# Kernel tuning notes

Hardware: AMD Instinct MI355X
Metric: run time of the kernel (lower is better)

Reference implementation:

```python
import jax, jax.numpy as jnp
import numpy as np

B = 32768
H = 512
NH = 8
EPS = 1e-5


def _glorot(key, shape):
    fan_in, fan_out = shape[-1], shape[0]
    lim = (6.0 / (fan_in + fan_out)) ** 0.5
    return jax.random.uniform(key, shape, jnp.float32, -lim, lim)


def setup_inputs() -> dict:
    key = jax.random.key(0)
    ks = jax.random.split(key, 32)
    d = {
        "graph_features": jax.random.normal(ks[0], (B, H), jnp.float32),
        "seq_features": jax.random.normal(ks[1], (B, H), jnp.float32),
        "tabular_features": jax.random.normal(ks[2], (B, H), jnp.float32),
    }
    i = 3
    for name in ("g2s", "s2g", "t2m"):
        d[f"{name}_w_in"] = _glorot(ks[i], (3 * H, H)); i += 1
        d[f"{name}_b_in"] = jnp.zeros((3 * H,), jnp.float32)
        d[f"{name}_w_out"] = _glorot(ks[i], (H, H)); i += 1
        d[f"{name}_b_out"] = jnp.zeros((H,), jnp.float32)
    for name in ("gate_g", "gate_s", "gate_t"):
        d[f"{name}_w"] = _glorot(ks[i], (H, 2 * H)); i += 1
        d[f"{name}_b"] = jnp.zeros((H,), jnp.float32)
    d["fc1_w"] = _glorot(ks[i], (2 * H, 3 * H)); i += 1
    d["fc1_b"] = jnp.zeros((2 * H,), jnp.float32)
    d["ln_g"] = jnp.ones((2 * H,), jnp.float32)
    d["ln_b"] = jnp.zeros((2 * H,), jnp.float32)
    d["fc2_w"] = _glorot(ks[i], (H, 2 * H)); i += 1
    d["fc2_b"] = jnp.zeros((H,), jnp.float32)
    return d


def _mha(q, k, v, w_in, b_in, w_out, b_out):
    # q: [B,Sq,H], k/v: [B,Sk,H]. PyTorch nn.MultiheadAttention math (eval mode).
    dh = H // NH
    qp = q @ w_in[:H].T + b_in[:H]
    kp = k @ w_in[H:2 * H].T + b_in[H:2 * H]
    vp = v @ w_in[2 * H:].T + b_in[2 * H:]
    qh = qp.reshape(qp.shape[0], qp.shape[1], NH, dh)
    kh = kp.reshape(kp.shape[0], kp.shape[1], NH, dh)
    vh = vp.reshape(vp.shape[0], vp.shape[1], NH, dh)
    scores = jnp.einsum("bqhd,bkhd->bhqk", qh, kh) / jnp.sqrt(jnp.float32(dh))
    attn = jax.nn.softmax(scores, axis=-1)
    out = jnp.einsum("bhqk,bkhd->bqhd", attn, vh).reshape(q.shape[0], q.shape[1], H)
    return out @ w_out.T + b_out


def reference(graph_features, seq_features, tabular_features,
              g2s_w_in, g2s_b_in, g2s_w_out, g2s_b_out,
              s2g_w_in, s2g_b_in, s2g_w_out, s2g_b_out,
              t2m_w_in, t2m_b_in, t2m_w_out, t2m_b_out,
              gate_g_w, gate_g_b, gate_s_w, gate_s_b, gate_t_w, gate_t_b,
              fc1_w, fc1_b, ln_g, ln_b, fc2_w, fc2_b):
    g = graph_features[:, None, :]   # [B,1,H]
    s = seq_features[:, None, :]
    t = tabular_features[:, None, :]

    graph_to_seq = _mha(s, g, g, g2s_w_in, g2s_b_in, g2s_w_out, g2s_b_out)
    seq_to_graph = _mha(g, s, s, s2g_w_in, s2g_b_in, s2g_w_out, s2g_b_out)

    graph_gate = jax.nn.sigmoid(jnp.concatenate([g, seq_to_graph], -1) @ gate_g_w.T + gate_g_b)
    seq_gate = jax.nn.sigmoid(jnp.concatenate([s, graph_to_seq], -1) @ gate_s_w.T + gate_s_b)
    gated_graph = g * graph_gate
    gated_seq = s * seq_gate

    multimodal = jnp.concatenate([gated_graph, gated_seq], axis=1)  # [B,2,H]
    t2m = _mha(multimodal, t, t, t2m_w_in, t2m_b_in, t2m_w_out, t2m_b_out)  # [B,2,H]

    tab_comb = jnp.concatenate([t, t2m.mean(axis=1, keepdims=True)], -1)
    tab_gate = jax.nn.sigmoid(tab_comb @ gate_t_w.T + gate_t_b)
    gated_tab = t * tab_gate

    allf = jnp.concatenate([gated_graph[:, 0], gated_seq[:, 0], gated_tab[:, 0]], -1)  # [B,3H]
    h = allf @ fc1_w.T + fc1_b
    mu = h.mean(-1, keepdims=True)
    var = ((h - mu) ** 2).mean(-1, keepdims=True)
    h = (h - mu) / jnp.sqrt(var + EPS) * ln_g + ln_b
    h = jax.nn.relu(h)
    return h @ fc2_w.T + fc2_b
```

## Files before the change

### kernel.cpp

```cpp
#include <hip/hip_runtime.h>
#include <stdint.h>
#include <stddef.h>

#define MROWS 32768
#define HDIM  512
#define CH    16384
#define BM 128
#define BN 128
#define BK 64

typedef __attribute__((ext_vector_type(8))) _Float16 half8;
typedef __attribute__((ext_vector_type(4))) _Float16 half4v;
typedef __attribute__((ext_vector_type(4))) float    f32x4;

static __device__ __forceinline__ void gld_lds16(const void* g, void* l) {
    __builtin_amdgcn_global_load_lds(
        (__attribute__((address_space(1))) void*)(uintptr_t)g,
        (__attribute__((address_space(3))) void*)(uint32_t)(uintptr_t)l,
        16, 0, 0);
}

struct CvtJob  { const float* src; _Float16* dst; int srcld4, dstld, rowlen4, rows; };
struct CvtJobs { CvtJob j[11]; };

__global__ __launch_bounds__(256)
void cvt_rows(CvtJobs J) {
    const CvtJob jb = J.j[blockIdx.y];
    const int row = blockIdx.x;
    if (row >= jb.rows) return;
    const float4* __restrict__ s = (const float4*)jb.src + (size_t)row * jb.srcld4;
    _Float16* __restrict__ d = jb.dst + (size_t)row * jb.dstld;
    for (int c = threadIdx.x; c < jb.rowlen4; c += 256) {
        const float4 v = s[c];
        half4v o = { (_Float16)v.x, (_Float16)v.y, (_Float16)v.z, (_Float16)v.w };
        *(half4v*)(d + c * 4) = o;
    }
}

__global__ __launch_bounds__(384)
void cvt_chunk3(const float* __restrict__ x0, const float* __restrict__ x1,
                const float* __restrict__ x2, _Float16* __restrict__ dst) {
    const int row = blockIdx.x;
    const int mod = threadIdx.x >> 7;
    const int c   = threadIdx.x & 127;
    const float* s = (mod == 0) ? x0 : (mod == 1) ? x1 : x2;
    const float4 v = ((const float4*)(s + (size_t)row * 512))[c];
    half4v o = { (_Float16)v.x, (_Float16)v.y, (_Float16)v.z, (_Float16)v.w };
    *(half4v*)(dst + (size_t)row * 1536 + mod * 512 + c * 4) = o;
}

struct TcvtArgs { const float* src[3]; _Float16* dst; };
__global__ __launch_bounds__(256)
void tcvt512(TcvtArgs a) {
    __shared__ float t[32][33];
    const int m = blockIdx.z;
    const float* __restrict__ src = a.src[m];
    _Float16* __restrict__ dst = a.dst + (size_t)m * HDIM * HDIM;
    const int bx = blockIdx.x * 32, by = blockIdx.y * 32;
    const int tx = threadIdx.x & 31, ty = threadIdx.x >> 5;
    #pragma unroll
    for (int q = 0; q < 4; ++q)
        t[ty + q * 8][tx] = src[(size_t)(by + ty + q * 8) * 512 + bx + tx];
    __syncthreads();
    #pragma unroll
    for (int q = 0; q < 4; ++q)
        dst[(size_t)(bx + ty + q * 8) * 512 + by + tx] = (_Float16)t[tx][ty + q * 8];
}

struct MvArgs { const float* W[3]; const float* x[3]; const float* b[3]; float* y; int ldw, woff; };
__global__ __launch_bounds__(256)
void mv3(MvArgs a) {
    const int m = blockIdx.y;
    const int i = blockIdx.x * 256 + threadIdx.x;
    const float* __restrict__ W = a.W[m] + (size_t)i * a.ldw + a.woff;
    const float* __restrict__ x = a.x[m];
    float s = a.b[m][i];
    for (int j = 0; j < 512; ++j) s += W[j] * x[j];
    a.y[m * 512 + i] = s;
}

struct GemmP {
    const void* A1;
    const _Float16* W; const float* bias; void* C;
    int K, ldA1, ldw, ldc, coff;
    int zsA, zsW, zsC;
};

template<int EPI, int OCC>
__global__ __launch_bounds__(256, OCC)
void gemm_k(GemmP p) {
    __shared__ __align__(16) unsigned char smem[32768];
    _Float16* Asm = (_Float16*)smem;
    _Float16* Bsm = (_Float16*)(smem + 16384);

    const int tid  = threadIdx.x;
    const int wid  = tid >> 6;
    const int lane = tid & 63;
    const int m0 = blockIdx.x * BM;
    const int n0 = blockIdx.y * BN;
    const ptrdiff_t zz = (ptrdiff_t)blockIdx.z;
    const _Float16* __restrict__ A1h = (const _Float16*)((const char*)p.A1 + zz * p.zsA);
    const _Float16* __restrict__ Wp  = (const _Float16*)((const char*)p.W + zz * p.zsW);
    char* Cz = (char*)p.C + zz * p.zsC;

    const int wr = (wid >> 1) * 64;
    const int wc = (wid & 1) * 64;
    const int l15 = lane & 15;
    const int lhi = lane >> 4;

    f32x4 acc[4][4] = {};

    for (int kt = 0; kt < p.K; kt += BK) {
        #pragma unroll
        for (int i = 0; i < 4; ++i) {
            const int seg = wid * 256 + i * 64 + lane;
            const int row = seg >> 3;
            const int ke  = (seg & 7) * 8;
            gld_lds16(Wp  + (size_t)(n0 + row) * p.ldw  + kt + ke, &Bsm[seg * 8]);
            gld_lds16(A1h + (size_t)(m0 + row) * p.ldA1 + kt + ke, &Asm[seg * 8]);
        }
        __syncthreads();
        #pragma unroll
        for (int kk = 0; kk < BK; kk += 32) {
            half8 fa[4], fb[4];
            #pragma unroll
            for (int i = 0; i < 4; ++i) {
                fa[i] = *(const half8*)&Asm[(wr + i * 16 + l15) * BK + kk + lhi * 8];
                fb[i] = *(const half8*)&Bsm[(wc + i * 16 + l15) * BK + kk + lhi * 8];
            }
            #pragma unroll
            for (int i = 0; i < 4; ++i)
                #pragma unroll
                for (int j = 0; j < 4; ++j)
                    acc[i][j] = __builtin_amdgcn_mfma_f32_16x16x32_f16(fa[i], fb[j], acc[i][j], 0, 0, 0);
        }
        __syncthreads();
    }

    if (EPI == 3) {
        float* Cf = (float*)smem;
        float* __restrict__ C = (float*)Cz;
        #pragma unroll
        for (int h = 0; h < 2; ++h) {
            if ((wr >> 6) == h) {
                #pragma unroll
                for (int j = 0; j < 4; ++j) {
                    const int col = wc + j * 16 + l15;
                    const float bia = p.bias ? p.bias[n0 + col] : 0.f;
                    #pragma unroll
                    for (int i = 0; i < 4; ++i)
                        #pragma unroll
                        for (int r = 0; r < 4; ++r)
                            Cf[(i * 16 + lhi * 4 + r) * 128 + col] = acc[i][j][r] + bia;
                }
            }
            __syncthreads();
            #pragma unroll
            for (int pph = 0; pph < 8; ++pph) {
                const int seg = pph * 256 + tid;
                const int row = seg >> 5, cs = seg & 31;
                const float4 v = *(const float4*)&Cf[row * 128 + cs * 4];
                *(float4*)&C[(size_t)(m0 + h * 64 + row) * p.ldc + n0 + cs * 4] = v;
            }
            __syncthreads();
        }
    } else {
        _Float16* Ct = (_Float16*)smem;
        #pragma unroll
        for (int j = 0; j < 4; ++j) {
            const int col = wc + j * 16 + l15;
            const float bia = (EPI == 2) ? 0.f : (p.bias ? p.bias[n0 + col] : 0.f);
            #pragma unroll
            for (int i = 0; i < 4; ++i)
                #pragma unroll
                for (int r = 0; r < 4; ++r) {
                    float v = acc[i][j][r] + bia;
                    if (EPI == 1) v = 1.f / (1.f + __expf(-v));
                    Ct[(wr + i * 16 + lhi * 4 + r) * 128 + col] = (_Float16)v;
                }
        }
        __syncthreads();
        _Float16* __restrict__ C = (_Float16*)Cz;
        #pragma unroll
        for (int pph = 0; pph < 8; ++pph) {
            const int seg = pph * 256 + tid;
            const int row = seg >> 4, cs = seg & 15;
            half8 hv = *(const half8*)&Ct[row * 128 + cs * 8];
            const size_t cidx = (size_t)(m0 + row) * p.ldc + p.coff + n0 + cs * 8;
            if (EPI == 1) {
                const half8 xv = *(const half8*)(A1h + (size_t)(m0 + row) * p.ldA1
                                                 + n0 + cs * 8);
                hv = hv * xv;
            }
            if (EPI == 2) { const half8 old = *(const half8*)&C[cidx]; hv = hv + old; }
            *(half8*)&C[cidx] = hv;
        }
    }
}

struct Gemm8P {
    const _Float16* A; const _Float16* W; const float* bias; void* C;
    int K, ldA, ldW, ldc, coff;
};

template<int EPI>
__global__ __launch_bounds__(512, 1)
void gemm8(Gemm8P p) {
    __shared__ __align__(16) unsigned char lds[131072];
    char* LA = (char*)lds;
    char* LB = (char*)lds + 65536;

    const int tid  = threadIdx.x;
    const int wid  = tid >> 6;
    const int lane = tid & 63;
    const int wm = wid >> 2;
    const int wn = wid & 3;
    const int l15 = lane & 15;
    const int lhi = lane >> 4;
    const int m0 = blockIdx.x * 256;
    const int n0 = blockIdx.y * 256;
    const _Float16* __restrict__ A = p.A;
    const _Float16* __restrict__ W = p.W;
    const int ldA = p.ldA, ldW = p.ldW;
    const int nT = p.K >> 6;

    f32x4 acc[8][4] = {};

    auto stageh = [&](const _Float16* src, int ld, int r0, char* base, int t, int kh) {
        const int q = t & 1;
        const int kt = t * 64 + kh * 32;
        char* dst = base + (size_t)(q * 2 + kh) * 16384;
        #pragma unroll
        for (int k = 0; k < 2; ++k) {
            const int j = tid + k * 512;
            const int row = j >> 2, i = j & 3;
            const int kc = i ^ ((row >> 1) & 3);
            gld_lds16(src + (size_t)(r0 + row) * ld + kt + kc * 8,
                      dst + (size_t)j * 16);
        }
    };
    #define STAGE8(t, kh) { stageh(A, ldA, m0, LA, (t), (kh)); stageh(W, ldW, n0, LB, (t), (kh)); }

    STAGE8(0, 0);
    STAGE8(0, 1);
    if (nT > 1) { STAGE8(1, 0); asm volatile("s_waitcnt vmcnt(8)" ::: "memory"); }
    else        {               asm volatile("s_waitcnt vmcnt(0)" ::: "memory"); }
    __builtin_amdgcn_s_barrier();
    asm volatile("" ::: "memory");

    for (int t = 0; t < nT; ++t) {
        const int q = t & 1;
        #pragma unroll
        for (int kh = 0; kh < 2; ++kh) {
            const char* ra = LA + (size_t)(q * 2 + kh) * 16384;
            const char* rb = LB + (size_t)(q * 2 + kh) * 16384;
            half8 fa[8], fb[4];
            #pragma unroll
            for (int nf = 0; nf < 4; ++nf) {
                const int row = wn * 64 + nf * 16 + l15;
                const int sl = lhi ^ ((row >> 1) & 3);
                fb[nf] = *(const half8*)(rb + ((size_t)row * 4 + sl) * 16);
            }
            #pragma unroll
            for (int mf = 0; mf < 8; ++mf) {
                const int row = wm * 128 + mf * 16 + l15;
                const int sl = lhi ^ ((row >> 1) & 3);
                fa[mf] = *(const half8*)(ra + ((size_t)row * 4 + sl) * 16);
            }
            if (kh == 0 && t + 1 < nT) STAGE8(t + 1, 1);
            if (kh == 1 && t + 2 < nT) STAGE8(t + 2, 0);
            __builtin_amdgcn_s_setprio(1);
            #pragma unroll
            for (int mf = 0; mf < 8; ++mf)
                #pragma unroll
                for (int nf = 0; nf < 4; ++nf)
                    acc[mf][nf] = __builtin_amdgcn_mfma_f32_16x16x32_f16(
                        fa[mf], fb[nf], acc[mf][nf], 0, 0, 0);
            __builtin_amdgcn_s_setprio(0);
            __builtin_amdgcn_sched_barrier(0);
            if (kh == 0) {
                if (t + 1 < nT) asm volatile("s_waitcnt vmcnt(8)" ::: "memory");
                else            asm volatile("s_waitcnt vmcnt(0)" ::: "memory");
            } else {
                if (t + 2 < nT)      asm volatile("s_waitcnt vmcnt(8)" ::: "memory");
                else if (t + 1 < nT) asm volatile("s_waitcnt vmcnt(4)" ::: "memory");
            }
            asm volatile("" ::: "memory");
            __builtin_amdgcn_s_barrier();
            asm volatile("" ::: "memory");
        }
    }

    if (EPI == 3) {
        float* Cf = (float*)lds;
        float* __restrict__ C = (float*)p.C;
        #pragma unroll
        for (int h = 0; h < 2; ++h) {
            if (wm == h) {
                #pragma unroll
                for (int mf = 0; mf < 8; ++mf)
                    #pragma unroll
                    for (int nf = 0; nf < 4; ++nf) {
                        const int col = wn * 64 + nf * 16 + l15;
                        const float bia = p.bias[n0 + col];
                        #pragma unroll
                        for (int r = 0; r < 4; ++r)
                            Cf[(mf * 16 + lhi * 4 + r) * 256 + col] = acc[mf][nf][r] + bia;
                    }
            }
            __syncthreads();
            #pragma unroll
            for (int it = 0; it < 16; ++it) {
                const int u = it * 512 + tid;
                const int row = u >> 6, cs = u & 63;
                const float4 v = *(const float4*)&Cf[row * 256 + cs * 4];
                *(float4*)&C[(size_t)(m0 + h * 128 + row) * p.ldc + n0 + cs * 4] = v;
            }
            __syncthreads();
        }
    } else {
        _Float16* Ct = (_Float16*)lds;
        _Float16* __restrict__ C = (_Float16*)p.C;
        #pragma unroll
        for (int mf = 0; mf < 8; ++mf)
            #pragma unroll
            for (int nf = 0; nf < 4; ++nf) {
                const int col = wn * 64 + nf * 16 + l15;
                const float bia = p.bias[n0 + col];
                #pragma unroll
                for (int r = 0; r < 4; ++r) {
                    float v = acc[mf][nf][r] + bia;
                    if (EPI == 1) v = 1.f / (1.f + __expf(-v));
                    Ct[(wm * 128 + mf * 16 + lhi * 4 + r) * 256 + col] = (_Float16)v;
                }
            }
        __syncthreads();
        #pragma unroll
        for (int it = 0; it < 16; ++it) {
            const int u = it * 512 + tid;
            const int row = u >> 5, cs = u & 31;
            half8 hv = *(const half8*)&Ct[row * 256 + cs * 8];
            if (EPI == 1) {
                const half8 xv = *(const half8*)(A + (size_t)(m0 + row) * ldA + n0 + cs * 8);
                hv = hv * xv;
            }
            *(half8*)&C[(size_t)(m0 + row) * p.ldc + p.coff + n0 + cs * 8] = hv;
        }
    }
}

__global__ __launch_bounds__(256)
void ln_relu(const _Float16* __restrict__ hin, _Float16* __restrict__ hout,
             const float* __restrict__ gamma, const float* __restrict__ beta) {
    const int row  = blockIdx.x * 4 + (threadIdx.x >> 6);
    const int lane = threadIdx.x & 63;
    const _Float16* hr = hin + (size_t)row * 1024;
    _Float16* ho = hout + (size_t)row * 1024;
    const half8 v0 = *(const half8*)(hr + lane * 8);
    const half8 v1 = *(const half8*)(hr + 512 + lane * 8);
    float f0[8], f1[8];
    float s = 0.f, s2 = 0.f;
    #pragma unroll
    for (int j = 0; j < 8; ++j) {
        f0[j] = (float)v0[j]; s += f0[j]; s2 += f0[j] * f0[j];
        f1[j] = (float)v1[j]; s += f1[j]; s2 += f1[j] * f1[j];
    }
    #pragma unroll
    for (int off = 32; off > 0; off >>= 1) {
        s  += __shfl_xor(s,  off, 64);
        s2 += __shfl_xor(s2, off, 64);
    }
    const float mean = s * (1.f / 1024.f);
    const float var  = s2 * (1.f / 1024.f) - mean * mean;
    const float rstd = rsqrtf(var + 1e-5f);
    half8 o0, o1;
    #pragma unroll
    for (int j = 0; j < 8; ++j) {
        const int i0 = lane * 8 + j, i1 = 512 + lane * 8 + j;
        const float av = (f0[j] - mean) * rstd * gamma[i0] + beta[i0];
        const float bv = (f1[j] - mean) * rstd * gamma[i1] + beta[i1];
        o0[j] = (_Float16)(av > 0.f ? av : 0.f);
        o1[j] = (_Float16)(bv > 0.f ? bv : 0.f);
    }
    *(half8*)(ho + lane * 8) = o0;
    *(half8*)(ho + 512 + lane * 8) = o1;
}

extern "C" void kernel_launch(void* const* d_in, const int* in_sizes, int n_in,
                              void* d_out, int out_size, void* d_ws, size_t ws_size,
                              hipStream_t stream)
{
    (void)in_sizes; (void)n_in; (void)out_size;
    const size_t HH = (size_t)HDIM * HDIM;

    _Float16* wsH   = (_Float16*)d_ws;
    _Float16* slotB = wsH;
    _Float16* Xch   = slotB + (size_t)CH * 1536;
    _Float16* Wouth = Xch   + (size_t)CH * 1536;
    _Float16* Wg2h  = Wouth + 3 * HH;
    _Float16* WvT   = Wg2h  + 3 * HH;
    _Float16* WcoT  = WvT   + 3 * HH;
    _Float16* Wbig  = WcoT  + 3 * HH;
    _Float16* Wc2   = Wbig  + 4 * HH;
    _Float16* fc1h  = Wc2   + 1 * HH;
    _Float16* fc2h  = fc1h  + 6 * HH;
    float*    bco   = (float*)(fc2h + 2 * HH);
    float*    beff  = bco + 3 * 512;
    _Float16* hws   = wsH;
    const size_t need = (size_t)((char*)(beff + 3 * 512) - (char*)d_ws);
    if (ws_size < need) return;

    const float* X[3] = { (const float*)d_in[0], (const float*)d_in[1], (const float*)d_in[2] };
    const int asrc[3] = { 1, 0, 2 };

    CvtJobs cj;
    for (int m = 0; m < 3; ++m) {
        cj.j[m]     = { (const float*)d_in[5 + 4 * m], Wouth + m * HH, 128, 512, 128, 512 };
        cj.j[3 + m] = { (const float*)d_in[15 + 2 * m] + 512, Wg2h + m * HH, 256, 512, 128, 512 };
    }
    cj.j[6]  = { (const float*)d_in[15], Wbig,                    256, 1024, 128, 512 };
    cj.j[7]  = { (const float*)d_in[17], Wbig + 512 * 1024 + 512, 256, 1024, 128, 512 };
    cj.j[8]  = { (const float*)d_in[19], Wc2,                     256, 512,  128, 512 };
    cj.j[9]  = { (const float*)d_in[21], fc1h, 384, 1536, 384, 1024 };
    cj.j[10] = { (const float*)d_in[25], fc2h, 256, 1024, 256, 512 };
    cvt_rows<<<dim3(1024, 11, 1), 256, 0, stream>>>(cj);

    TcvtArgs ta;
    for (int m = 0; m < 3; ++m) ta.src[m] = (const float*)d_in[3 + 4 * m] + 2 * HH;
    ta.dst = WvT;
    tcvt512<<<dim3(16, 16, 3), 256, 0, stream>>>(ta);

    MvArgs mv;
    for (int m = 0; m < 3; ++m) {
        mv.W[m] = (const float*)d_in[5 + 4 * m];
        mv.x[m] = (const float*)d_in[4 + 4 * m] + 2 * HDIM;
        mv.b[m] = (const float*)d_in[6 + 4 * m];
    }
    mv.y = bco; mv.ldw = 512; mv.woff = 0;
    mv3<<<dim3(2, 3, 1), 256, 0, stream>>>(mv);

    GemmP p;
    p.bias = nullptr; p.coff = 0;
    p.zsA = p.zsW = p.zsC = 0;

    p.A1 = WvT; p.ldA1 = 512;
    p.W = Wouth; p.ldw = 512;
    p.C = WcoT; p.ldc = 512;
    p.K = 512;
    p.zsA = (int)(HH * 2); p.zsW = (int)(HH * 2); p.zsC = (int)(HH * 2);
    gemm_k<0, 4><<<dim3(4, 4, 3), 256, 0, stream>>>(p);

    p.A1 = Wg2h; p.zsA = (int)(HH * 2);
    p.W = WcoT + HH; p.zsW = -(int)(HH * 2);
    p.C = Wbig + 512; p.ldc = 1024; p.zsC = (int)((512 * 1024 - 512) * 2);
    gemm_k<0, 4><<<dim3(4, 4, 2), 256, 0, stream>>>(p);

    p.A1 = Wg2h + 2 * HH; p.zsA = 0;
    p.W = WcoT + 2 * HH; p.zsW = 0;
    p.C = Wc2; p.ldc = 512; p.zsC = 0;
    gemm_k<2, 4><<<dim3(4, 4, 1), 256, 0, stream>>>(p);

    for (int m = 0; m < 3; ++m) {
        mv.W[m] = (const float*)d_in[15 + 2 * m];
        mv.x[m] = bco + asrc[m] * 512;
        mv.b[m] = (const float*)d_in[16 + 2 * m];
    }
    mv.y = beff; mv.ldw = 1024; mv.woff = 512;
    mv3<<<dim3(2, 3, 1), 256, 0, stream>>>(mv);

    _Float16* hbuf = (_Float16*)d_out;
    Gemm8P g8;
    for (int c = 0; c < 2; ++c) {
        const size_t roff = (size_t)c * CH;

        cvt_chunk3<<<dim3(CH, 1, 1), 384, 0, stream>>>(
            X[0] + roff * HDIM, X[1] + roff * HDIM, X[2] + roff * HDIM, Xch);

        g8.A = Xch; g8.ldA = 1536;
        g8.W = Wbig; g8.ldW = 1024;
        g8.bias = beff;
        g8.C = slotB; g8.ldc = 1536; g8.coff = 0;
        g8.K = 1024;
        gemm8<1><<<dim3(CH / 256, 4, 1), 512, 0, stream>>>(g8);

        p.A1 = Xch + 1024; p.ldA1 = 1536;
        p.W = Wc2; p.ldw = 512;
        p.bias = beff + 1024;
        p.C = slotB; p.ldc = 1536; p.coff = 1024;
        p.K = 512; p.zsA = p.zsW = p.zsC = 0;
        gemm_k<1, 4><<<dim3(CH / BM, 4, 1), 256, 0, stream>>>(p);

        g8.A = slotB; g8.ldA = 1536;
        g8.W = fc1h; g8.ldW = 1536;
        g8.bias = (const float*)d_in[22];
        g8.C = hbuf + roff * 1024; g8.ldc = 1024; g8.coff = 0;
        g8.K = 1536;
        gemm8<0><<<dim3(CH / 256, 4, 1), 512, 0, stream>>>(g8);
    }

    ln_relu<<<dim3(MROWS / 4, 1, 1), 256, 0, stream>>>(
        hbuf, hws, (const float*)d_in[23], (const float*)d_in[24]);

    g8.A = hws; g8.ldA = 1024;
    g8.W = fc2h; g8.ldW = 1024;
    g8.bias = (const float*)d_in[26];
    g8.C = d_out; g8.ldc = HDIM; g8.coff = 0;
    g8.K = 1024;
    gemm8<3><<<dim3(MROWS / 256, HDIM / 256, 1), 512, 0, stream>>>(g8);
}
```

Measured before the change: 457.2 us.

## Restructure GEMM main loop into one barrier per K-tile with interleaved fragment loads

Replaces the two-half-step K loop, which had a barrier and partial vmcnt waits after each 32-wide half, with one full 64-wide K tile per iteration. Both halves of the next tile are prefetched at once, and LDS fragment reads are interleaved with four MFMA blocks of 4x4. This halves the barriers and keeps fewer fragments live, to cut register pressure and sync stalls. In exchange the prefetch distance shrinks from about 1.5 tiles to one, and the full vmcnt(0) wait at the end of each tile may expose global-load latency.

Measured after the change: 455.0 us. About the same (-0.5%).

```diff
diff --git a/kernel.cpp b/kernel.cpp
--- a/kernel.cpp
+++ b/kernel.cpp
@@ -243,52 +243,95 @@
 
     STAGE8(0, 0);
     STAGE8(0, 1);
-    if (nT > 1) { STAGE8(1, 0); asm volatile("s_waitcnt vmcnt(8)" ::: "memory"); }
-    else        {               asm volatile("s_waitcnt vmcnt(0)" ::: "memory"); }
+    asm volatile("s_waitcnt vmcnt(0)" ::: "memory");
     __builtin_amdgcn_s_barrier();
     asm volatile("" ::: "memory");
 
     for (int t = 0; t < nT; ++t) {
         const int q = t & 1;
-        #pragma unroll
-        for (int kh = 0; kh < 2; ++kh) {
-            const char* ra = LA + (size_t)(q * 2 + kh) * 16384;
-            const char* rb = LB + (size_t)(q * 2 + kh) * 16384;
-            half8 fa[8], fb[4];
-            #pragma unroll
-            for (int nf = 0; nf < 4; ++nf) {
-                const int row = wn * 64 + nf * 16 + l15;
-                const int sl = lhi ^ ((row >> 1) & 3);
-                fb[nf] = *(const half8*)(rb + ((size_t)row * 4 + sl) * 16);
-            }
-            #pragma unroll
-            for (int mf = 0; mf < 8; ++mf) {
-                const int row = wm * 128 + mf * 16 + l15;
-                const int sl = lhi ^ ((row >> 1) & 3);
-                fa[mf] = *(const half8*)(ra + ((size_t)row * 4 + sl) * 16);
-            }
-            if (kh == 0 && t + 1 < nT) STAGE8(t + 1, 1);
-            if (kh == 1 && t + 2 < nT) STAGE8(t + 2, 0);
-            __builtin_amdgcn_s_setprio(1);
-            #pragma unroll
-            for (int mf = 0; mf < 8; ++mf)
-                #pragma unroll
-                for (int nf = 0; nf < 4; ++nf)
-                    acc[mf][nf] = __builtin_amdgcn_mfma_f32_16x16x32_f16(
-                        fa[mf], fb[nf], acc[mf][nf], 0, 0, 0);
-            __builtin_amdgcn_s_setprio(0);
-            __builtin_amdgcn_sched_barrier(0);
-            if (kh == 0) {
-                if (t + 1 < nT) asm volatile("s_waitcnt vmcnt(8)" ::: "memory");
-                else            asm volatile("s_waitcnt vmcnt(0)" ::: "memory");
-            } else {
-                if (t + 2 < nT)      asm volatile("s_waitcnt vmcnt(8)" ::: "memory");
-                else if (t + 1 < nT) asm volatile("s_waitcnt vmcnt(4)" ::: "memory");
-            }
-            asm volatile("" ::: "memory");
-            __builtin_amdgcn_s_barrier();
-            asm volatile("" ::: "memory");
-        }
+        const char* ra0 = LA + (size_t)(q * 2 + 0) * 16384;
+        const char* ra1 = LA + (size_t)(q * 2 + 1) * 16384;
+        const char* rb0 = LB + (size_t)(q * 2 + 0) * 16384;
+        const char* rb1 = LB + (size_t)(q * 2 + 1) * 16384;
+        half8 faA[4], faB[4], fb0[4], fb1[4];
+
+        #pragma unroll
+        for (int nf = 0; nf < 4; ++nf) {
+            const int row = wn * 64 + nf * 16 + l15;
+            const int sl = lhi ^ ((row >> 1) & 3);
+            fb0[nf] = *(const half8*)(rb0 + ((size_t)row * 4 + sl) * 16);
+        }
+        #pragma unroll
+        for (int mi = 0; mi < 4; ++mi) {
+            const int row = wm * 128 + mi * 16 + l15;
+            const int sl = lhi ^ ((row >> 1) & 3);
+            faA[mi] = *(const half8*)(ra0 + ((size_t)row * 4 + sl) * 16);
+        }
+        if (t + 1 < nT) { STAGE8(t + 1, 0); STAGE8(t + 1, 1); }
+
+        #pragma unroll
+        for (int mi = 0; mi < 4; ++mi) {
+            const int row = wm * 128 + (4 + mi) * 16 + l15;
+            const int sl = lhi ^ ((row >> 1) & 3);
+            faB[mi] = *(const half8*)(ra0 + ((size_t)row * 4 + sl) * 16);
+        }
+        __builtin_amdgcn_s_setprio(1);
+        #pragma unroll
+        for (int mi = 0; mi < 4; ++mi)
+            #pragma unroll
+            for (int nf = 0; nf < 4; ++nf)
+                acc[mi][nf] = __builtin_amdgcn_mfma_f32_16x16x32_f16(
+                    faA[mi], fb0[nf], acc[mi][nf], 0, 0, 0);
+        __builtin_amdgcn_s_setprio(0);
+
+        #pragma unroll
+        for (int nf = 0; nf < 4; ++nf) {
+            const int row = wn * 64 + nf * 16 + l15;
+            const int sl = lhi ^ ((row >> 1) & 3);
+            fb1[nf] = *(const half8*)(rb1 + ((size_t)row * 4 + sl) * 16);
+        }
+        #pragma unroll
+        for (int mi = 0; mi < 4; ++mi) {
+            const int row = wm * 128 + mi * 16 + l15;
+            const int sl = lhi ^ ((row >> 1) & 3);
+            faA[mi] = *(const half8*)(ra1 + ((size_t)row * 4 + sl) * 16);
+        }
+        __builtin_amdgcn_s_setprio(1);
+        #pragma unroll
+        for (int mi = 0; mi < 4; ++mi)
+            #pragma unroll
+            for (int nf = 0; nf < 4; ++nf)
+                acc[4 + mi][nf] = __builtin_amdgcn_mfma_f32_16x16x32_f16(
+                    faB[mi], fb0[nf], acc[4 + mi][nf], 0, 0, 0);
+        __builtin_amdgcn_s_setprio(0);
+
+        #pragma unroll
+        for (int mi = 0; mi < 4; ++mi) {
+            const int row = wm * 128 + (4 + mi) * 16 + l15;
+            const int sl = lhi ^ ((row >> 1) & 3);
+            faB[mi] = *(const half8*)(ra1 + ((size_t)row * 4 + sl) * 16);
+        }
+        __builtin_amdgcn_s_setprio(1);
+        #pragma unroll
+        for (int mi = 0; mi < 4; ++mi)
+            #pragma unroll
+            for (int nf = 0; nf < 4; ++nf)
+                acc[mi][nf] = __builtin_amdgcn_mfma_f32_16x16x32_f16(
+                    faA[mi], fb1[nf], acc[mi][nf], 0, 0, 0);
+        __builtin_amdgcn_s_setprio(0);
+
+        __builtin_amdgcn_s_setprio(1);
+        #pragma unroll
+        for (int mi = 0; mi < 4; ++mi)
+            #pragma unroll
+            for (int nf = 0; nf < 4; ++nf)
+                acc[4 + mi][nf] = __builtin_amdgcn_mfma_f32_16x16x32_f16(
+                    faB[mi], fb1[nf], acc[4 + mi][nf], 0, 0, 0);
+        __builtin_amdgcn_s_setprio(0);
+
+        asm volatile("s_waitcnt vmcnt(0)" ::: "memory");
+        __builtin_amdgcn_s_barrier();
+        asm volatile("" ::: "memory");
     }
 
     if (EPI == 3) {
```
